# Optimization experiments

Measured on AMD Instinct MI355X. Metric: run time of the kernel, lower is better.

Reference implementation:

```python
import jax, jax.numpy as jnp
import numpy as np


def conv3x3(x, w, b):
    # x: [B,1,H,W], w: [1,1,3,3] (OIHW), b: [1]; stride 1, padding 1
    y = jax.lax.conv_general_dilated(x, w, (1, 1), 'SAME',
                                     dimension_numbers=('NCHW', 'OIHW', 'NCHW'))
    return y + b[0]


def avg_pool(x, k):
    B, C, H, W = x.shape
    return x.reshape(B, C, H // k, k, W // k, k).mean(axis=(3, 5))


def nearest_up(x, k):
    # nearest-neighbor upsample by integer factor k (matches torch 'nearest')
    return jnp.repeat(jnp.repeat(x, k, axis=2), k, axis=3)


def conv1x1(x, w):
    # x: [B,3,H,W], w: [1,3,1,1] -> [B,1,H,W]
    return jnp.einsum('bchw,oc->bohw', x, w[:, :, 0, 0])


def setup_inputs() -> dict:
    key = jax.random.key(0)
    ks = jax.random.split(key, 16)
    B, H, W = 8, 512, 512
    std = 0.005
    inp = {
        'x':          jax.random.normal(ks[0], (B, 1, H, W), jnp.float32),
        'downSample': jax.random.normal(ks[1], (B, 1, H // 2, W // 2), jnp.float32),
        'upSample':   jax.random.normal(ks[2], (B, 1, 2 * H, 2 * W), jnp.float32),
        'BU':         jax.random.normal(ks[3], (B, 1, H, W), jnp.float32),
        'BUdown':     jax.random.normal(ks[4], (B, 1, H // 2, W // 2), jnp.float32),
        'BUup':       jax.random.normal(ks[5], (B, 1, 2 * H, 2 * W), jnp.float32),
        'convAx': std * jax.random.normal(ks[6], (1, 1, 3, 3), jnp.float32),
        'biasx':  std * jax.random.normal(ks[7], (1,), jnp.float32),
        'convAd': std * jax.random.normal(ks[8], (1, 1, 3, 3), jnp.float32),
        'biasd':  std * jax.random.normal(ks[9], (1,), jnp.float32),
        'convAu': std * jax.random.normal(ks[10], (1, 1, 3, 3), jnp.float32),
        'biasu':  std * jax.random.normal(ks[11], (1,), jnp.float32),
        'conv1x1_x': std * jax.random.normal(ks[12], (1, 3, 1, 1), jnp.float32),
        'conv1x1_d': std * jax.random.normal(ks[13], (1, 3, 1, 1), jnp.float32),
        'conv1x1_u': std * jax.random.normal(ks[14], (1, 3, 1, 1), jnp.float32),
    }
    return inp


def reference(x, downSample, upSample, BU, BUdown, BUup,
              convAx, biasx, convAd, biasd, convAu, biasu,
              conv1x1_x, conv1x1_d, conv1x1_u):
    # 5 iterations of conv3x3 + residual add + clamp(-1,1) per pyramid level
    for _ in range(5):
        x = jnp.clip(conv3x3(x, convAx, biasx) + BU, -1.0, 1.0)
        downSample = jnp.clip(conv3x3(downSample, convAd, biasd) + BUdown, -1.0, 1.0)
        upSample = jnp.clip(conv3x3(upSample, convAu, biasu) + BUup, -1.0, 1.0)
    # cross-scale fusion: resample all three levels to each level and concat
    newx = jnp.concatenate([avg_pool(upSample, 2), x, nearest_up(downSample, 2)], axis=1)
    newUp = jnp.concatenate([upSample, nearest_up(x, 2), nearest_up(downSample, 4)], axis=1)
    newDown = jnp.concatenate([avg_pool(upSample, 4), avg_pool(x, 2), downSample], axis=1)
    x_out = conv1x1(newx, conv1x1_x)
    down_out = conv1x1(newDown, conv1x1_d)
    up_out = conv1x1(newUp, conv1x1_u)
    return (x_out, down_out, up_out)
```

## Files before the change

kernel.cpp:

```cpp
#include <hip/hip_runtime.h>

#define NBATCH 8
#define TW 64
#define TH 32
#define SROWS 42
#define SQUADS 20
#define STRDQ 80
#define NPAIRS 20
#define NSTRIP 180
#define NTHR 192

__device__ __forceinline__ int lofs(int R, int q) {
    int rot = (3 * (R >> 1)) % 20;
    int p = q + rot;
    if (p >= 20) p -= 20;
    return R * STRDQ + (p << 2);
}

__device__ __forceinline__ void acc_row(float4& v, float L, float4 m, float R,
                                        float ka, float kb, float kc) {
    v.x += ka * L   + kb * m.x + kc * m.y;
    v.y += ka * m.x + kb * m.y + kc * m.z;
    v.z += ka * m.y + kb * m.z + kc * m.w;
    v.w += ka * m.z + kb * m.w + kc * R;
}

__device__ __forceinline__ void clamp_mask(float4& v, float4 pm) {
    v.x = __builtin_amdgcn_fmed3f(v.x, -1.0f, 1.0f) * pm.x;
    v.y = __builtin_amdgcn_fmed3f(v.y, -1.0f, 1.0f) * pm.y;
    v.z = __builtin_amdgcn_fmed3f(v.z, -1.0f, 1.0f) * pm.z;
    v.w = __builtin_amdgcn_fmed3f(v.w, -1.0f, 1.0f) * pm.w;
}

__global__ __launch_bounds__(NTHR, 4) void conv5_all(
    const float* __restrict__ srcU, const float* __restrict__ buU,
    const float* __restrict__ wtU, const float* __restrict__ bsU,
    const float* __restrict__ srcX, const float* __restrict__ buX,
    const float* __restrict__ wtX, const float* __restrict__ bsX,
    const float* __restrict__ srcD, const float* __restrict__ buD,
    const float* __restrict__ wtD, const float* __restrict__ bsD,
    float* __restrict__ dstU, float* __restrict__ dstX, float* __restrict__ dstD)
{
    __shared__ __align__(16) float bufA[SROWS * STRDQ];
    __shared__ __align__(16) float bufB[SROWS * STRDQ];

    const int tid = threadIdx.x;
    const int blk = blockIdx.x;

    const float* src; const float* BU; const float* wt; const float* bs;
    float* dst; int HW; int tx, ty, b;
    if (blk < 4096) {
        src = srcU; BU = buU; wt = wtU; bs = bsU; dst = dstU; HW = 1024;
        b = blk >> 9; int rem = blk & 511; ty = rem >> 4; tx = rem & 15;
    } else if (blk < 5120) {
        int t = blk - 4096;
        src = srcX; BU = buX; wt = wtX; bs = bsX; dst = dstX; HW = 512;
        b = t >> 7; int rem = t & 127; ty = rem >> 3; tx = rem & 7;
    } else {
        int t = blk - 5120;
        src = srcD; BU = buD; wt = wtD; bs = bsD; dst = dstD; HW = 256;
        b = t >> 5; int rem = t & 31; ty = rem >> 2; tx = rem & 3;
    }
    const int bh0 = ty * TH, bw0 = tx * TW;
    const long base = (long)b * HW * HW;

    for (int s = tid; s < SROWS * SQUADS; s += NTHR) {
        int r = s / SQUADS, cq = s - r * SQUADS;
        int gh = bh0 + r - 5;
        int gw = bw0 + (cq << 2) - 8;
        float4 v = {0.0f, 0.0f, 0.0f, 0.0f};
        if ((unsigned)gh < (unsigned)HW) {
            const float* gp = src + base + (long)gh * HW + gw;
            if (gw >= 0 && gw + 3 < HW) {
                v = *(const float4*)gp;
            } else {
                if ((unsigned)(gw + 0) < (unsigned)HW) v.x = gp[0];
                if ((unsigned)(gw + 1) < (unsigned)HW) v.y = gp[1];
                if ((unsigned)(gw + 2) < (unsigned)HW) v.z = gp[2];
                if ((unsigned)(gw + 3) < (unsigned)HW) v.w = gp[3];
            }
        }
        *(float4*)&bufA[lofs(r, cq)] = v;
    }
    for (int s = tid; s < 120; s += NTHR) {
        int r, q;
        if (s < 40)      { r = (s < 20) ? 0 : 41; q = s % 20; }
        else             { int s2 = s - 40; r = 1 + (s2 >> 1); q = (s2 & 1) ? 19 : 0; }
        float4 z = {0.0f, 0.0f, 0.0f, 0.0f};
        *(float4*)&bufB[lofs(r, q)] = z;
    }

    const float k00 = wt[0], k01 = wt[1], k02 = wt[2];
    const float k10 = wt[3], k11 = wt[4], k12 = wt[5];
    const float k20 = wt[6], k21 = wt[7], k22 = wt[8];
    const float bias = bs[0];

    const bool act = (tid < NSTRIP);
    int rp = 0, j = 0;
    {
        int g = (0x75426310u >> ((tid & 7) << 2)) & 0xF;
        int need = tid >> 3;
        for (int r_ = (g & 1); r_ < NPAIRS; r_ += 2) {
            int j0 = ((g - 3 * r_) & 7) >> 1;
            int c = (j0 == 0) ? 3 : 2;
            if (need < c) { rp = r_; j = j0 + 4 * need; break; }
            need -= c;
        }
    }

    int rdo[4][4];
    #pragma unroll
    for (int r = 0; r < 4; ++r)
        #pragma unroll
        for (int c = 0; c < 4; ++c)
            rdo[r][c] = lofs(2 * rp + r, 2 * j + c);
    int wro[2][2];
    #pragma unroll
    for (int i = 0; i < 2; ++i) {
        wro[i][0] = lofs(2 * rp + 1 + i, 2 * j + 1);
        wro[i][1] = lofs(2 * rp + 1 + i, 2 * j + 2);
    }

    float4 pm0[2], pm1[2];
    float hf[2];
    #pragma unroll
    for (int i = 0; i < 2; ++i) {
        int gh = bh0 + 2 * rp - 4 + i;
        hf[i] = (act && (unsigned)gh < (unsigned)HW) ? 1.0f : 0.0f;
        float* p0 = (float*)&pm0[i]; float* p1 = (float*)&pm1[i];
        #pragma unroll
        for (int k = 0; k < 4; ++k) {
            p0[k] = hf[i] * (((unsigned)(bw0 + 8 * j - 4 + k) < (unsigned)HW) ? 1.0f : 0.0f);
            p1[k] = hf[i] * (((unsigned)(bw0 + 8 * j + k)     < (unsigned)HW) ? 1.0f : 0.0f);
        }
    }
    float4 bu0[2], bu1[2];
    #pragma unroll
    for (int i = 0; i < 2; ++i) {
        int gh = bh0 + 2 * rp - 4 + i;
        bool hok = (hf[i] != 0.0f);
        int gw0 = bw0 + 8 * j - 4;
        const float* bp = BU + base + (long)gh * HW + gw0;
        if (hok && gw0 >= 0 && gw0 + 7 < HW) {
            float4 a = *(const float4*)bp;
            float4 c = *(const float4*)(bp + 4);
            bu0[i] = {a.x + bias, a.y + bias, a.z + bias, a.w + bias};
            bu1[i] = {c.x + bias, c.y + bias, c.z + bias, c.w + bias};
        } else {
            float* b0 = (float*)&bu0[i]; float* b1 = (float*)&bu1[i];
            #pragma unroll
            for (int k = 0; k < 4; ++k) {
                int w0 = gw0 + k;
                int w1 = gw0 + 4 + k;
                b0[k] = (hok && (unsigned)w0 < (unsigned)HW) ? (bp[k] + bias)     : 0.0f;
                b1[k] = (hok && (unsigned)w1 < (unsigned)HW) ? (bp[k + 4] + bias) : 0.0f;
            }
        }
    }

    float4 prev0[2], prev1[2];

    auto step = [&](const float* __restrict__ cs, float* __restrict__ ns,
                    bool first, bool last) {
        __syncthreads();
        if (act) {
            float4 q[4][4];
            #pragma unroll
            for (int r = 0; r < 4; ++r) {
                q[r][0] = *(const float4*)(cs + rdo[r][0]);
                q[r][3] = *(const float4*)(cs + rdo[r][3]);
            }
            q[0][1] = *(const float4*)(cs + rdo[0][1]);
            q[0][2] = *(const float4*)(cs + rdo[0][2]);
            q[3][1] = *(const float4*)(cs + rdo[3][1]);
            q[3][2] = *(const float4*)(cs + rdo[3][2]);
            if (first) {
                q[1][1] = *(const float4*)(cs + rdo[1][1]);
                q[1][2] = *(const float4*)(cs + rdo[1][2]);
                q[2][1] = *(const float4*)(cs + rdo[2][1]);
                q[2][2] = *(const float4*)(cs + rdo[2][2]);
            } else {
                q[1][1] = prev0[0];
                q[1][2] = prev1[0];
                q[2][1] = prev0[1];
                q[2][2] = prev1[1];
            }
            __builtin_amdgcn_s_setprio(1);
            #pragma unroll
            for (int i = 0; i < 2; ++i) {
                float4 v0 = bu0[i];
                float4 v1 = bu1[i];
                acc_row(v0, q[i][0].w,     q[i][1],     q[i][2].x,     k00, k01, k02);
                acc_row(v0, q[i + 1][0].w, q[i + 1][1], q[i + 1][2].x, k10, k11, k12);
                acc_row(v0, q[i + 2][0].w, q[i + 2][1], q[i + 2][2].x, k20, k21, k22);
                acc_row(v1, q[i][1].w,     q[i][2],     q[i][3].x,     k00, k01, k02);
                acc_row(v1, q[i + 1][1].w, q[i + 1][2], q[i + 1][3].x, k10, k11, k12);
                acc_row(v1, q[i + 2][1].w, q[i + 2][2], q[i + 2][3].x, k20, k21, k22);
                clamp_mask(v0, pm0[i]);
                clamp_mask(v1, pm1[i]);
                if (!last) {
                    prev0[i] = v0;
                    prev1[i] = v1;
                    *(float4*)(ns + wro[i][0]) = v0;
                    *(float4*)(ns + wro[i][1]) = v1;
                } else {
                    int r = 2 * rp - 4 + i;
                    if ((unsigned)r < (unsigned)TH) {
                        float* dp = dst + base + (long)(bh0 + r) * HW + bw0 + 8 * j;
                        if (j >= 1) *(float4*)(dp - 4) = v0;
                        if (j <= 7) *(float4*)(dp)     = v1;
                    }
                }
            }
            __builtin_amdgcn_s_setprio(0);
        }
    };

    step(bufA, bufB, true,  false);
    step(bufB, bufA, false, false);
    step(bufA, bufB, false, false);
    step(bufB, bufA, false, false);
    step(bufA, bufB, false, true);
}

__global__ __launch_bounds__(256) void fuse_all(
    const float* __restrict__ X,
    const float* __restrict__ D,
    const float* __restrict__ U,
    const float* __restrict__ cx,
    const float* __restrict__ cd,
    const float* __restrict__ cu,
    float* __restrict__ xo, float* __restrict__ dno, float* __restrict__ upo)
{
    const int total = NBATCH << 16;
    int idx = blockIdx.x * blockDim.x + threadIdx.x;
    if (idx >= total) return;
    int wd = idx & 255;
    int hd = (idx >> 8) & 255;
    int b  = idx >> 16;

    const float cx0 = cx[0], cx1 = cx[1], cx2 = cx[2];
    const float cd0 = cd[0], cd1 = cd[1], cd2 = cd[2];
    const float cu0 = cu[0], cu1 = cu[1], cu2 = cu[2];

    int ub = (b << 20) + ((hd << 2) << 10) + (wd << 2);
    float4 u0 = *(const float4*)&U[ub];
    float4 u1 = *(const float4*)&U[ub + 1024];
    float4 u2 = *(const float4*)&U[ub + 2048];
    float4 u3 = *(const float4*)&U[ub + 3072];
    int xb = (b << 18) + ((hd << 1) << 9) + (wd << 1);
    float2 x0 = *(const float2*)&X[xb];
    float2 x1 = *(const float2*)&X[xb + 512];
    float dv = D[idx];

    float p00 = 0.25f * (u0.x + u0.y + u1.x + u1.y);
    float p01 = 0.25f * (u0.z + u0.w + u1.z + u1.w);
    float p10 = 0.25f * (u2.x + u2.y + u3.x + u3.y);
    float p11 = 0.25f * (u2.z + u2.w + u3.z + u3.w);
    float pu4 = 0.25f * (p00 + p01 + p10 + p11);
    float px2 = 0.25f * (x0.x + x0.y + x1.x + x1.y);

    dno[idx] = cd0 * pu4 + cd1 * px2 + cd2 * dv;

    float2 xo0, xo1;
    xo0.x = cx0 * p00 + cx1 * x0.x + cx2 * dv;
    xo0.y = cx0 * p01 + cx1 * x0.y + cx2 * dv;
    xo1.x = cx0 * p10 + cx1 * x1.x + cx2 * dv;
    xo1.y = cx0 * p11 + cx1 * x1.y + cx2 * dv;
    *(float2*)&xo[xb]       = xo0;
    *(float2*)&xo[xb + 512] = xo1;

    float4 o0, o1, o2, o3;
    o0.x = cu0 * u0.x + cu1 * x0.x + cu2 * dv;
    o0.y = cu0 * u0.y + cu1 * x0.x + cu2 * dv;
    o0.z = cu0 * u0.z + cu1 * x0.y + cu2 * dv;
    o0.w = cu0 * u0.w + cu1 * x0.y + cu2 * dv;
    o1.x = cu0 * u1.x + cu1 * x0.x + cu2 * dv;
    o1.y = cu0 * u1.y + cu1 * x0.x + cu2 * dv;
    o1.z = cu0 * u1.z + cu1 * x0.y + cu2 * dv;
    o1.w = cu0 * u1.w + cu1 * x0.y + cu2 * dv;
    o2.x = cu0 * u2.x + cu1 * x1.x + cu2 * dv;
    o2.y = cu0 * u2.y + cu1 * x1.x + cu2 * dv;
    o2.z = cu0 * u2.z + cu1 * x1.y + cu2 * dv;
    o2.w = cu0 * u2.w + cu1 * x1.y + cu2 * dv;
    o3.x = cu0 * u3.x + cu1 * x1.x + cu2 * dv;
    o3.y = cu0 * u3.y + cu1 * x1.x + cu2 * dv;
    o3.z = cu0 * u3.z + cu1 * x1.y + cu2 * dv;
    o3.w = cu0 * u3.w + cu1 * x1.y + cu2 * dv;
    *(float4*)&upo[ub]        = o0;
    *(float4*)&upo[ub + 1024] = o1;
    *(float4*)&upo[ub + 2048] = o2;
    *(float4*)&upo[ub + 3072] = o3;
}

extern "C" void kernel_launch(void* const* d_in, const int* in_sizes, int n_in,
                              void* d_out, int out_size, void* d_ws, size_t ws_size,
                              hipStream_t stream)
{
    const float* x    = (const float*)d_in[0];
    const float* down = (const float*)d_in[1];
    const float* up   = (const float*)d_in[2];
    const float* BUx  = (const float*)d_in[3];
    const float* BUd  = (const float*)d_in[4];
    const float* BUu  = (const float*)d_in[5];
    const float* wAx  = (const float*)d_in[6];
    const float* bx   = (const float*)d_in[7];
    const float* wAd  = (const float*)d_in[8];
    const float* bd   = (const float*)d_in[9];
    const float* wAu  = (const float*)d_in[10];
    const float* bu   = (const float*)d_in[11];
    const float* c1x  = (const float*)d_in[12];
    const float* c1d  = (const float*)d_in[13];
    const float* c1u  = (const float*)d_in[14];

    float* out = (float*)d_out;
    float* ws  = (float*)d_ws;

    const int NX = NBATCH * 512 * 512;
    const int ND = NBATCH * 256 * 256;

    float* wsX = ws;
    float* wsD = ws + NX;
    float* wsU = ws + NX + ND;
    float* outX = out;
    float* outD = out + NX;
    float* outU = out + NX + ND;

    conv5_all<<<5376, NTHR, 0, stream>>>(
        up,   BUu, wAu, bu,
        x,    BUx, wAx, bx,
        down, BUd, wAd, bd,
        wsU, wsX, wsD);

    fuse_all<<<(ND + 255) / 256, 256, 0, stream>>>(wsX, wsD, wsU, c1x, c1d, c1u,
                                                   outX, outD, outU);
}
```

Baseline: 207.2 us.

## Use single LDS buffer with extra barrier and raise occupancy bound to eight

Replaces the double-buffered LDS ping-pong with one in-place buffer. A second barrier separates the read phase from the write phase in each step, and only the needed edge scalars are loaded instead of full float4 edge quads. Halving LDS use and raising the launch_bounds blocks-per-CU hint from 4 to 8 aims for higher occupancy, at the cost of an extra __syncthreads per iteration and tighter register limits that could cause spills.

```diff
diff --git a/kernel.cpp b/kernel.cpp
--- a/kernel.cpp
+++ b/kernel.cpp
@@ -32,7 +32,7 @@
     v.w = __builtin_amdgcn_fmed3f(v.w, -1.0f, 1.0f) * pm.w;
 }
 
-__global__ __launch_bounds__(NTHR, 4) void conv5_all(
+__global__ __launch_bounds__(NTHR, 8) void conv5_all(
     const float* __restrict__ srcU, const float* __restrict__ buU,
     const float* __restrict__ wtU, const float* __restrict__ bsU,
     const float* __restrict__ srcX, const float* __restrict__ buX,
@@ -41,8 +41,7 @@
     const float* __restrict__ wtD, const float* __restrict__ bsD,
     float* __restrict__ dstU, float* __restrict__ dstX, float* __restrict__ dstD)
 {
-    __shared__ __align__(16) float bufA[SROWS * STRDQ];
-    __shared__ __align__(16) float bufB[SROWS * STRDQ];
+    __shared__ __align__(16) float buf[SROWS * STRDQ];
 
     const int tid = threadIdx.x;
     const int blk = blockIdx.x;
@@ -80,14 +79,7 @@
                 if ((unsigned)(gw + 3) < (unsigned)HW) v.w = gp[3];
             }
         }
-        *(float4*)&bufA[lofs(r, cq)] = v;
-    }
-    for (int s = tid; s < 120; s += NTHR) {
-        int r, q;
-        if (s < 40)      { r = (s < 20) ? 0 : 41; q = s % 20; }
-        else             { int s2 = s - 40; r = 1 + (s2 >> 1); q = (s2 & 1) ? 19 : 0; }
-        float4 z = {0.0f, 0.0f, 0.0f, 0.0f};
-        *(float4*)&bufB[lofs(r, q)] = z;
+        *(float4*)&buf[lofs(r, cq)] = v;
     }
 
     const float k00 = wt[0], k01 = wt[1], k02 = wt[2];
@@ -108,17 +100,14 @@
         }
     }
 
-    int rdo[4][4];
+    int rdm[4][2];
+    int e0o[4], e3o[4];
     #pragma unroll
-    for (int r = 0; r < 4; ++r)
-        #pragma unroll
-        for (int c = 0; c < 4; ++c)
-            rdo[r][c] = lofs(2 * rp + r, 2 * j + c);
-    int wro[2][2];
-    #pragma unroll
-    for (int i = 0; i < 2; ++i) {
-        wro[i][0] = lofs(2 * rp + 1 + i, 2 * j + 1);
-        wro[i][1] = lofs(2 * rp + 1 + i, 2 * j + 2);
+    for (int r = 0; r < 4; ++r) {
+        rdm[r][0] = lofs(2 * rp + r, 2 * j + 1);
+        rdm[r][1] = lofs(2 * rp + r, 2 * j + 2);
+        e0o[r]    = lofs(2 * rp + r, 2 * j) + 3;
+        e3o[r]    = lofs(2 * rp + r, 2 * j + 3);
     }
 
     float4 pm0[2], pm1[2];
@@ -160,49 +149,50 @@
 
     float4 prev0[2], prev1[2];
 
-    auto step = [&](const float* __restrict__ cs, float* __restrict__ ns,
-                    bool first, bool last) {
+    auto step = [&](bool first, bool last) {
         __syncthreads();
+        float4 qm[4][2];
+        float  e0[4], e3[4];
         if (act) {
-            float4 q[4][4];
             #pragma unroll
             for (int r = 0; r < 4; ++r) {
-                q[r][0] = *(const float4*)(cs + rdo[r][0]);
-                q[r][3] = *(const float4*)(cs + rdo[r][3]);
-            }
-            q[0][1] = *(const float4*)(cs + rdo[0][1]);
-            q[0][2] = *(const float4*)(cs + rdo[0][2]);
-            q[3][1] = *(const float4*)(cs + rdo[3][1]);
-            q[3][2] = *(const float4*)(cs + rdo[3][2]);
+                e0[r] = buf[e0o[r]];
+                e3[r] = buf[e3o[r]];
+            }
+            qm[0][0] = *(const float4*)(buf + rdm[0][0]);
+            qm[0][1] = *(const float4*)(buf + rdm[0][1]);
+            qm[3][0] = *(const float4*)(buf + rdm[3][0]);
+            qm[3][1] = *(const float4*)(buf + rdm[3][1]);
             if (first) {
-                q[1][1] = *(const float4*)(cs + rdo[1][1]);
-                q[1][2] = *(const float4*)(cs + rdo[1][2]);
-                q[2][1] = *(const float4*)(cs + rdo[2][1]);
-                q[2][2] = *(const float4*)(cs + rdo[2][2]);
+                qm[1][0] = *(const float4*)(buf + rdm[1][0]);
+                qm[1][1] = *(const float4*)(buf + rdm[1][1]);
+                qm[2][0] = *(const float4*)(buf + rdm[2][0]);
+                qm[2][1] = *(const float4*)(buf + rdm[2][1]);
             } else {
-                q[1][1] = prev0[0];
-                q[1][2] = prev1[0];
-                q[2][1] = prev0[1];
-                q[2][2] = prev1[1];
-            }
+                qm[1][0] = prev0[0]; qm[1][1] = prev1[0];
+                qm[2][0] = prev0[1]; qm[2][1] = prev1[1];
+            }
+        }
+        if (!last) __syncthreads();
+        if (act) {
             __builtin_amdgcn_s_setprio(1);
             #pragma unroll
             for (int i = 0; i < 2; ++i) {
                 float4 v0 = bu0[i];
                 float4 v1 = bu1[i];
-                acc_row(v0, q[i][0].w,     q[i][1],     q[i][2].x,     k00, k01, k02);
-                acc_row(v0, q[i + 1][0].w, q[i + 1][1], q[i + 1][2].x, k10, k11, k12);
-                acc_row(v0, q[i + 2][0].w, q[i + 2][1], q[i + 2][2].x, k20, k21, k22);
-                acc_row(v1, q[i][1].w,     q[i][2],     q[i][3].x,     k00, k01, k02);
-                acc_row(v1, q[i + 1][1].w, q[i + 1][2], q[i + 1][3].x, k10, k11, k12);
-                acc_row(v1, q[i + 2][1].w, q[i + 2][2], q[i + 2][3].x, k20, k21, k22);
+                acc_row(v0, e0[i],         qm[i][0],     qm[i][1].x,     k00, k01, k02);
+                acc_row(v0, e0[i + 1],     qm[i + 1][0], qm[i + 1][1].x, k10, k11, k12);
+                acc_row(v0, e0[i + 2],     qm[i + 2][0], qm[i + 2][1].x, k20, k21, k22);
+                acc_row(v1, qm[i][0].w,     qm[i][1],     e3[i],         k00, k01, k02);
+                acc_row(v1, qm[i + 1][0].w, qm[i + 1][1], e3[i + 1],     k10, k11, k12);
+                acc_row(v1, qm[i + 2][0].w, qm[i + 2][1], e3[i + 2],     k20, k21, k22);
                 clamp_mask(v0, pm0[i]);
                 clamp_mask(v1, pm1[i]);
                 if (!last) {
                     prev0[i] = v0;
                     prev1[i] = v1;
-                    *(float4*)(ns + wro[i][0]) = v0;
-                    *(float4*)(ns + wro[i][1]) = v1;
+                    *(float4*)(buf + rdm[1 + i][0]) = v0;
+                    *(float4*)(buf + rdm[1 + i][1]) = v1;
                 } else {
                     int r = 2 * rp - 4 + i;
                     if ((unsigned)r < (unsigned)TH) {
@@ -216,11 +206,11 @@
         }
     };
 
-    step(bufA, bufB, true,  false);
-    step(bufB, bufA, false, false);
-    step(bufA, bufB, false, false);
-    step(bufB, bufA, false, false);
-    step(bufA, bufB, false, true);
+    step(true,  false);
+    step(false, false);
+    step(false, false);
+    step(false, false);
+    step(false, true);
 }
 
 __global__ __launch_bounds__(256) void fuse_all(
```

Result: slower. 458.5 us (+121.3%).
